# Kernel tuning notes

Hardware: AMD Instinct MI355X
Metric: run time of the kernel (lower is better)

The kernel has to match this reference:

```python
import jax, jax.numpy as jnp
import numpy as np

N_NODES = 100000
N_EDGES = 1600000
DIM_IN, DIM_H, DIM_OUT = 15, 128, 1


def _glorot(key, shape):
    fan_in, fan_out = shape[0], shape[1]
    lim = float(np.sqrt(6.0 / (fan_in + fan_out)))
    return jax.random.uniform(key, shape, jnp.float32, -lim, lim)


def setup_inputs() -> dict:
    key = jax.random.key(0)
    ks = jax.random.split(key, 12)
    x = jax.random.normal(ks[0], (N_NODES, DIM_IN), jnp.float32)
    edge_index = jax.random.randint(ks[1], (2, N_EDGES), 0, N_NODES, jnp.int64)
    # PyG SAGEConv: out = lin_l(mean_aggr(x_src)) + lin_r(x_dst); bias lives in lin_l.
    # Weights stored as [in, out] for x @ W.
    params = {
        "W1l": _glorot(ks[2], (DIM_IN, DIM_H)), "W1r": _glorot(ks[3], (DIM_IN, DIM_H)), "b1": jnp.zeros((DIM_H,), jnp.float32),
        "W2l": _glorot(ks[4], (DIM_H, DIM_H)), "W2r": _glorot(ks[5], (DIM_H, DIM_H)), "b2": jnp.zeros((DIM_H,), jnp.float32),
        "W3l": _glorot(ks[6], (DIM_H, DIM_OUT)), "W3r": _glorot(ks[7], (DIM_H, DIM_OUT)), "b3": jnp.zeros((DIM_OUT,), jnp.float32),
    }
    return {"x": x, "edge_index": edge_index, **params}


def _sage_conv(h, src, dst, deg_inv, Wl, Wr, b):
    # mean-aggregate source features at destination nodes
    agg = jax.ops.segment_sum(h[src], dst, num_segments=N_NODES) * deg_inv
    return agg @ Wl + h @ Wr + b


def reference(x, edge_index, W1l, W1r, b1, W2l, W2r, b2, W3l, W3r, b3):
    src, dst = edge_index[0], edge_index[1]
    deg = jax.ops.segment_sum(jnp.ones((src.shape[0],), x.dtype), dst, num_segments=N_NODES)
    deg_inv = (1.0 / jnp.maximum(deg, 1.0))[:, None]  # [N,1]
    h = jax.nn.relu(_sage_conv(x, src, dst, deg_inv, W1l, W1r, b1))  # dropout is identity in eval
    h = jax.nn.relu(_sage_conv(h, src, dst, deg_inv, W2l, W2r, b2))
    h = _sage_conv(h, src, dst, deg_inv, W3l, W3r, b3)
    return h
```

## Files before the change

kernel.cpp:

```cpp
#include <hip/hip_runtime.h>
#include <hip/hip_bf16.h>

constexpr int N = 100000;
constexpr int E = 1600000;
constexpr int DIN = 15;
constexpr int DH  = 128;
constexpr int K2  = 256;
constexpr int NPAD = 100032;

constexpr int CHUNK     = 8192;
constexpr int NBLK_P1   = (E + CHUNK - 1) / CHUNK;
constexpr int BKT_NODES = 512;
constexpr int NBKT      = (N + BKT_NODES - 1) / BKT_NODES;
constexpr int LREC_CAP  = 10240;

typedef short short8 __attribute__((ext_vector_type(8)));
typedef float f32x4  __attribute__((ext_vector_type(4)));

__device__ __forceinline__ unsigned short f2bf_rne(float f) {
    unsigned u = __float_as_uint(f);
    u += 0x7fffu + ((u >> 16) & 1u);
    return (unsigned short)(u >> 16);
}
__device__ __forceinline__ float bf2f(unsigned short h) {
    return __uint_as_float(((unsigned)h) << 16);
}
__device__ __forceinline__ float bflo(unsigned u) { return __uint_as_float(u << 16); }
__device__ __forceinline__ float bfhi(unsigned u) { return __uint_as_float(u & 0xffff0000u); }

__global__ __launch_bounds__(256) void k_prep(const float* __restrict__ x,
                                              const float* __restrict__ W2l,
                                              const float* __restrict__ W2r,
                                              const float* __restrict__ W1l,
                                              const float* __restrict__ W1r,
                                              unsigned int* __restrict__ xb32,
                                              unsigned short* __restrict__ Wthi,
                                              unsigned short* __restrict__ Wtlo,
                                              unsigned short* __restrict__ Wt1hi,
                                              unsigned short* __restrict__ Wt1lo,
                                              unsigned int* __restrict__ agg1b,
                                              int* __restrict__ btot) {
    int id = blockIdx.x * 256 + threadIdx.x;
    if (id < NBKT) btot[id] = 0;
    if (id < DH * K2) {
        int col = id & 127;
        int k   = id >> 7;
        float wv = (k < DH) ? W2l[k * DH + col] : W2r[(k - DH) * DH + col];
        unsigned short hi = f2bf_rne(wv);
        unsigned short lo = f2bf_rne(wv - bf2f(hi));
        Wthi[col * K2 + k] = hi;
        Wtlo[col * K2 + k] = lo;
        return;
    }
    int xid = id - DH * K2;
    if (xid < NPAD * 8) {
        int n = xid >> 3, d2 = xid & 7;
        unsigned v = 0;
        if (n < N) {
            int d0 = 2 * d2, d1 = 2 * d2 + 1;
            float v0 = x[n * DIN + d0];
            float v1 = (d1 < DIN) ? x[n * DIN + d1] : 0.f;
            v = (unsigned)f2bf_rne(v0) | ((unsigned)f2bf_rne(v1) << 16);
        }
        xb32[xid] = v;
        return;
    }
    int wid = xid - NPAD * 8;
    if (wid < DH * 32) {
        int col = wid >> 5;
        int k   = wid & 31;
        float wv = 0.f;
        if (k < DIN)                 wv = W1l[k * DH + col];
        else if (k >= 16 && k < 31)  wv = W1r[(k - 16) * DH + col];
        unsigned short hi = f2bf_rne(wv);
        unsigned short lo = f2bf_rne(wv - bf2f(hi));
        Wt1hi[col * 32 + k] = hi;
        Wt1lo[col * 32 + k] = lo;
        return;
    }
    int aid = wid - DH * 32;
    if (aid < (NPAD - N) * 8) agg1b[N * 8 + aid] = 0;
}

__global__ __launch_bounds__(1024) void k_p1(const int* __restrict__ src,
                                             const int* __restrict__ dst,
                                             unsigned int* __restrict__ bsorted,
                                             int* __restrict__ offg,
                                             int* __restrict__ btot) {
    __shared__ int hist[256];
    __shared__ int scn[256];
    __shared__ int fill[256];
    __shared__ unsigned int srt[CHUNK];
    const int t   = threadIdx.x;
    const int blk = blockIdx.x;
    const int e0  = blk * CHUNK;
    if (t < 256) hist[t] = 0;
    __syncthreads();
#pragma unroll
    for (int j = 0; j < CHUNK / 1024; ++j) {
        int i = e0 + t + j * 1024;
        if (i < E) atomicAdd(&hist[dst[i] >> 9], 1);
    }
    __syncthreads();
    if (t < 256) {
        if (t < NBKT && hist[t]) atomicAdd(&btot[t], hist[t]);
        scn[t] = hist[t];
    }
    __syncthreads();
    for (int d = 1; d < 256; d <<= 1) {
        int v = (t >= d && t < 256) ? scn[t - d] : 0;
        __syncthreads();
        if (t < 256) scn[t] += v;
        __syncthreads();
    }
    if (t < 256) {
        int excl = (t == 0) ? 0 : scn[t - 1];
        fill[t] = excl;
        if (t < NBKT) offg[blk * (NBKT + 1) + t] = excl;
        if (t == 0)   offg[blk * (NBKT + 1) + NBKT] = scn[NBKT - 1];
    }
    __syncthreads();
#pragma unroll
    for (int j = 0; j < CHUNK / 1024; ++j) {
        int i = e0 + t + j * 1024;
        if (i < E) {
            int dv = dst[i];
            int b  = dv >> 9;
            int pos = atomicAdd(&fill[b], 1);
            srt[pos] = ((unsigned)(dv & 511) << 17) | (unsigned)src[i];
        }
    }
    __syncthreads();
    for (int i = t; i < CHUNK; i += 1024) bsorted[e0 + i] = srt[i];
}

__global__ __launch_bounds__(1024) void k_p2(const unsigned int* __restrict__ bsorted,
                                             const int* __restrict__ offg,
                                             const int* __restrict__ btot,
                                             int* __restrict__ csr,
                                             int* __restrict__ rowptr,
                                             float* __restrict__ deg_inv) {
    __shared__ unsigned int lrec[LREC_CAP];
    __shared__ int cum[NBLK_P1 + 1];
    __shared__ int runstart[NBLK_P1];
    __shared__ int ldeg[BKT_NODES];
    __shared__ int lrp[BKT_NODES];
    __shared__ int lfill[BKT_NODES];
    __shared__ int pscan[256];
    __shared__ int sbs;

    const int b = blockIdx.x;
    const int t = threadIdx.x;

    if (t < 256) pscan[t] = (t < NBKT) ? btot[t] : 0;
    __syncthreads();
    for (int d = 1; d < 256; d <<= 1) {
        int v = (t >= d && t < 256) ? pscan[t - d] : 0;
        __syncthreads();
        if (t < 256) pscan[t] += v;
        __syncthreads();
    }
    if (t == 0) sbs = (b == 0) ? 0 : pscan[b - 1];
    __syncthreads();
    const int bs = sbs;

    int cnt_blk = 0;
    if (t < NBLK_P1) {
        int o0 = offg[t * (NBKT + 1) + b];
        cnt_blk = offg[t * (NBKT + 1) + b + 1] - o0;
        runstart[t] = o0;
    }
    __syncthreads();
    if (t < 256) pscan[t] = cnt_blk;
    __syncthreads();
    for (int d = 1; d < 256; d <<= 1) {
        int v = (t >= d && t < 256) ? pscan[t - d] : 0;
        __syncthreads();
        if (t < 256) pscan[t] += v;
        __syncthreads();
    }
    if (t < NBLK_P1) cum[t] = (t == 0) ? 0 : pscan[t - 1];
    if (t == 0) cum[NBLK_P1] = pscan[NBLK_P1 - 1];
    if (t < BKT_NODES) ldeg[t] = 0;
    __syncthreads();

    int total = cum[NBLK_P1];
    if (total > LREC_CAP) total = LREC_CAP;

    for (int i = t; i < total; i += 1024) {
        int lo = 0, hi = NBLK_P1;
        while (hi - lo > 1) {
            int mid = (lo + hi) >> 1;
            if (cum[mid] <= i) lo = mid; else hi = mid;
        }
        lrec[i] = bsorted[lo * CHUNK + runstart[lo] + (i - cum[lo])];
    }
    __syncthreads();

    for (int i = t; i < total; i += 1024) atomicAdd(&ldeg[lrec[i] >> 17], 1);
    __syncthreads();

    int p0 = 0, p1 = 0;
    if (t < 256) {
        p0 = ldeg[2 * t];
        p1 = ldeg[2 * t + 1];
        pscan[t] = p0 + p1;
    }
    __syncthreads();
    for (int d = 1; d < 256; d <<= 1) {
        int v = (t >= d && t < 256) ? pscan[t - d] : 0;
        __syncthreads();
        if (t < 256) pscan[t] += v;
        __syncthreads();
    }
    if (t < 256) {
        int pairbase = (t == 0) ? 0 : pscan[t - 1];
        lrp[2 * t]     = pairbase;
        lrp[2 * t + 1] = pairbase + p0;
    }
    if (t < BKT_NODES) lfill[t] = 0;
    __syncthreads();

    for (int i = t; i < total; i += 1024) {
        unsigned rec = lrec[i];
        int ld  = rec >> 17;
        int pos = lrp[ld] + atomicAdd(&lfill[ld], 1);
        csr[bs + pos] = (int)(rec & 0x1ffff);
    }
    if (t < BKT_NODES) {
        int g = b * BKT_NODES + t;
        if (g < N) {
            rowptr[g]  = bs + lrp[t];
            deg_inv[g] = 1.0f / fmaxf((float)ldeg[t], 1.0f);
        }
    }
    if (b == NBKT - 1 && t == 0) rowptr[N] = E;
}

__global__ __launch_bounds__(256) void k_agg1(const int* __restrict__ rowptr,
                                              const int* __restrict__ csr,
                                              const uint2* __restrict__ xb2,
                                              const float* __restrict__ deg_inv,
                                              uint2* __restrict__ agg1b2) {
    const int tid = threadIdx.x;
    const int l4  = tid & 3;
    const int gb4 = (tid & 63) & 60;
    const int n = blockIdx.x * 64 + (tid >> 2);
    if (n >= N) return;
    const int lo = rowptr[n], hi = rowptr[n + 1];
    float a0 = 0.f, a1 = 0.f, a2 = 0.f, a3 = 0.f;
    float b0 = 0.f, b1 = 0.f, b2 = 0.f, b3 = 0.f;
    float c0 = 0.f, c1 = 0.f, c2 = 0.f, c3 = 0.f;
    float d0 = 0.f, d1 = 0.f, d2 = 0.f, d3 = 0.f;
    int base = lo;
    for (; base + 8 <= hi; base += 8) {
        int e0 = csr[base + l4];
        int e1 = csr[base + 4 + l4];
        int s0 = __shfl(e0, gb4 + 0), s1 = __shfl(e0, gb4 + 1);
        int s2 = __shfl(e0, gb4 + 2), s3 = __shfl(e0, gb4 + 3);
        int s4 = __shfl(e1, gb4 + 0), s5 = __shfl(e1, gb4 + 1);
        int s6 = __shfl(e1, gb4 + 2), s7 = __shfl(e1, gb4 + 3);
        uint2 u0 = xb2[s0 * 4 + l4];
        uint2 u1 = xb2[s1 * 4 + l4];
        uint2 u2 = xb2[s2 * 4 + l4];
        uint2 u3 = xb2[s3 * 4 + l4];
        uint2 u4 = xb2[s4 * 4 + l4];
        uint2 u5 = xb2[s5 * 4 + l4];
        uint2 u6 = xb2[s6 * 4 + l4];
        uint2 u7 = xb2[s7 * 4 + l4];
        a0 += bflo(u0.x); a1 += bfhi(u0.x); a2 += bflo(u0.y); a3 += bfhi(u0.y);
        b0 += bflo(u1.x); b1 += bfhi(u1.x); b2 += bflo(u1.y); b3 += bfhi(u1.y);
        c0 += bflo(u2.x); c1 += bfhi(u2.x); c2 += bflo(u2.y); c3 += bfhi(u2.y);
        d0 += bflo(u3.x); d1 += bfhi(u3.x); d2 += bflo(u3.y); d3 += bfhi(u3.y);
        a0 += bflo(u4.x); a1 += bfhi(u4.x); a2 += bflo(u4.y); a3 += bfhi(u4.y);
        b0 += bflo(u5.x); b1 += bfhi(u5.x); b2 += bflo(u5.y); b3 += bfhi(u5.y);
        c0 += bflo(u6.x); c1 += bfhi(u6.x); c2 += bflo(u6.y); c3 += bfhi(u6.y);
        d0 += bflo(u7.x); d1 += bfhi(u7.x); d2 += bflo(u7.y); d3 += bfhi(u7.y);
    }
    int cnt = hi - base;
    if (cnt > 0) {
        int e0 = (base + l4 < hi) ? csr[base + l4] : 0;
        int e1 = (base + 4 + l4 < hi) ? csr[base + 4 + l4] : 0;
        int jm = min(cnt, 4);
        for (int j = 0; j < jm; ++j) {
            int s = __shfl(e0, gb4 + j);
            uint2 u = xb2[s * 4 + l4];
            a0 += bflo(u.x); a1 += bfhi(u.x); a2 += bflo(u.y); a3 += bfhi(u.y);
        }
        for (int j = 4; j < cnt; ++j) {
            int s = __shfl(e1, gb4 + j - 4);
            uint2 u = xb2[s * 4 + l4];
            b0 += bflo(u.x); b1 += bfhi(u.x); b2 += bflo(u.y); b3 += bfhi(u.y);
        }
    }
    const float di = deg_inv[n];
    float v0 = ((a0 + b0) + (c0 + d0)) * di;
    float v1 = ((a1 + b1) + (c1 + d1)) * di;
    float v2 = ((a2 + b2) + (c2 + d2)) * di;
    float v3 = ((a3 + b3) + (c3 + d3)) * di;
    uint2 o;
    o.x = (unsigned)f2bf_rne(v0) | ((unsigned)f2bf_rne(v1) << 16);
    o.y = (unsigned)f2bf_rne(v2) | ((unsigned)f2bf_rne(v3) << 16);
    agg1b2[n * 4 + l4] = o;
}

__global__ __launch_bounds__(256) void k_h1(const uint4* __restrict__ agg1b4,
                                            const uint4* __restrict__ xb4,
                                            const unsigned short* __restrict__ Wt1hi,
                                            const unsigned short* __restrict__ Wt1lo,
                                            const float* __restrict__ b1,
                                            unsigned int* __restrict__ h1hi32) {
    __shared__ __align__(16) unsigned short sA[4 * 64 * 8];
    __shared__ __align__(16) unsigned short sH[64 * 128];
    __shared__ float sb[DH];

    const int tid   = threadIdx.x;
    const int node0 = blockIdx.x * 64;

    if (tid < DH) sb[tid] = b1[tid];
    {
        int c = tid >> 6;
        int n = tid & 63;
        uint4 v = (c < 2) ? agg1b4[(node0 + n) * 2 + c]
                          : xb4[(node0 + n) * 2 + (c - 2)];
        *(uint4*)&sA[(c * 64 + (n ^ c)) * 8] = v;
    }
    __syncthreads();

    const int w    = tid >> 6;
    const int lane = tid & 63;
    const int cg   = lane & 15;
    const int lg   = lane >> 4;

    f32x4 acc[4][2];
#pragma unroll
    for (int a = 0; a < 4; ++a)
#pragma unroll
        for (int b = 0; b < 2; ++b)
            acc[a][b] = (f32x4){0.f, 0.f, 0.f, 0.f};

    short8 bh0 = *(const short8*)&Wt1hi[(w * 32 + 0 * 16 + cg) * 32 + lg * 8];
    short8 bh1 = *(const short8*)&Wt1hi[(w * 32 + 1 * 16 + cg) * 32 + lg * 8];
    short8 bl0 = *(const short8*)&Wt1lo[(w * 32 + 0 * 16 + cg) * 32 + lg * 8];
    short8 bl1 = *(const short8*)&Wt1lo[(w * 32 + 1 * 16 + cg) * 32 + lg * 8];

#pragma unroll
    for (int rt = 0; rt < 4; ++rt) {
        const int n = rt * 16 + cg;
        short8 a = *(const short8*)&sA[(lg * 64 + (n ^ lg)) * 8];
        acc[rt][0] = __builtin_amdgcn_mfma_f32_16x16x32_bf16(a, bh0, acc[rt][0], 0, 0, 0);
        acc[rt][0] = __builtin_amdgcn_mfma_f32_16x16x32_bf16(a, bl0, acc[rt][0], 0, 0, 0);
        acc[rt][1] = __builtin_amdgcn_mfma_f32_16x16x32_bf16(a, bh1, acc[rt][1], 0, 0, 0);
        acc[rt][1] = __builtin_amdgcn_mfma_f32_16x16x32_bf16(a, bl1, acc[rt][1], 0, 0, 0);
    }

#pragma unroll
    for (int rt = 0; rt < 4; ++rt)
#pragma unroll
        for (int ci = 0; ci < 2; ++ci) {
            const int col = w * 32 + ci * 16 + cg;
            const float bb = sb[col];
#pragma unroll
            for (int reg = 0; reg < 4; ++reg) {
                const int row = rt * 16 + lg * 4 + reg;
                sH[row * 128 + col] = f2bf_rne(fmaxf(acc[rt][ci][reg] + bb, 0.f));
            }
        }
    __syncthreads();
    const uint4* sH4 = (const uint4*)sH;
    uint4* out4 = (uint4*)h1hi32;
#pragma unroll
    for (int it = 0; it < 4; ++it) {
        int idx = tid + it * 256;
        out4[node0 * 16 + idx] = sH4[idx];
    }
}

__global__ __launch_bounds__(256) void k_agg2(const int* __restrict__ rowptr,
                                              const int* __restrict__ csr,
                                              const unsigned int* __restrict__ h1b,
                                              const float* __restrict__ deg_inv,
                                              unsigned int* __restrict__ agg2b) {
    const int lane = threadIdx.x & 63;
    const int n = blockIdx.x * 4 + (threadIdx.x >> 6);
    if (n >= N) return;
    const int lo = rowptr[n], hi = rowptr[n + 1];
    float a0x = 0.f, a0y = 0.f, a1x = 0.f, a1y = 0.f;
    float a2x = 0.f, a2y = 0.f, a3x = 0.f, a3y = 0.f;
    float a4x = 0.f, a4y = 0.f, a5x = 0.f, a5y = 0.f;
    float a6x = 0.f, a6y = 0.f, a7x = 0.f, a7y = 0.f;
    for (int base = lo; base < hi; base += 64) {
        const int cnt = min(64, hi - base);
        int e = (base + lane < hi) ? csr[base + lane] : 0;
        int j = 0;
        for (; j + 8 <= cnt; j += 8) {
            int s0 = __shfl(e, j + 0), s1 = __shfl(e, j + 1);
            int s2 = __shfl(e, j + 2), s3 = __shfl(e, j + 3);
            int s4 = __shfl(e, j + 4), s5 = __shfl(e, j + 5);
            int s6 = __shfl(e, j + 6), s7 = __shfl(e, j + 7);
            unsigned u0 = h1b[s0 * 64 + lane];
            unsigned u1 = h1b[s1 * 64 + lane];
            unsigned u2 = h1b[s2 * 64 + lane];
            unsigned u3 = h1b[s3 * 64 + lane];
            unsigned u4 = h1b[s4 * 64 + lane];
            unsigned u5 = h1b[s5 * 64 + lane];
            unsigned u6 = h1b[s6 * 64 + lane];
            unsigned u7 = h1b[s7 * 64 + lane];
            a0x += bflo(u0); a0y += bfhi(u0);
            a1x += bflo(u1); a1y += bfhi(u1);
            a2x += bflo(u2); a2y += bfhi(u2);
            a3x += bflo(u3); a3y += bfhi(u3);
            a4x += bflo(u4); a4y += bfhi(u4);
            a5x += bflo(u5); a5y += bfhi(u5);
            a6x += bflo(u6); a6y += bfhi(u6);
            a7x += bflo(u7); a7y += bfhi(u7);
        }
        for (; j < cnt; ++j) {
            int s = __shfl(e, j);
            unsigned u = h1b[s * 64 + lane];
            a0x += bflo(u); a0y += bfhi(u);
        }
    }
    const float di = deg_inv[n];
    float vx = (((a0x + a1x) + (a2x + a3x)) + ((a4x + a5x) + (a6x + a7x))) * di;
    float vy = (((a0y + a1y) + (a2y + a3y)) + ((a4y + a5y) + (a6y + a7y))) * di;
    agg2b[n * 64 + lane] = (unsigned)f2bf_rne(vx) | ((unsigned)f2bf_rne(vy) << 16);
}

__global__ __launch_bounds__(256) void k_h2pr(const unsigned int* __restrict__ agg2b,
                                              const unsigned int* __restrict__ h1hi32,
                                              const unsigned short* __restrict__ Wthi,
                                              const unsigned short* __restrict__ Wtlo,
                                              const float* __restrict__ b2,
                                              const float* __restrict__ W3l,
                                              const float* __restrict__ W3r,
                                              float* __restrict__ p,
                                              float* __restrict__ r) {
    __shared__ __align__(16) unsigned short sA[32 * 64 * 8];
    __shared__ float sb2[DH], sW3l[DH], sW3r[DH];
    __shared__ float sPP[4 * 64], sPR[4 * 64];

    const int tid   = threadIdx.x;
    const int node0 = blockIdx.x * 64;

    if (tid < DH) {
        sb2[tid]  = b2[tid];
        sW3l[tid] = W3l[tid];
        sW3r[tid] = W3r[tid];
    }

#pragma unroll
    for (int it = 0; it < 4; ++it) {
        int idx = tid + it * 256;
        int n   = idx >> 4;
        int cp  = idx & 15;
        uint4 va = *(const uint4*)&agg2b[(node0 + n) * 64 + cp * 4];
        *(uint4*)&sA[(cp * 64 + (n ^ (cp & 7))) * 8] = va;
    }
#pragma unroll
    for (int it = 0; it < 4; ++it) {
        int idx = tid + it * 256;
        int n   = idx >> 4;
        int cp  = idx & 15;
        int c   = 16 + cp;
        uint4 vh = *(const uint4*)&h1hi32[(node0 + n) * 64 + cp * 4];
        *(uint4*)&sA[(c * 64 + (n ^ (cp & 7))) * 8] = vh;
    }
    __syncthreads();

    const int w    = tid >> 6;
    const int lane = tid & 63;
    const int cg   = lane & 15;
    const int lg   = lane >> 4;

    f32x4 acc[4][2];
#pragma unroll
    for (int a = 0; a < 4; ++a)
#pragma unroll
        for (int b = 0; b < 2; ++b)
            acc[a][b] = (f32x4){0.f, 0.f, 0.f, 0.f};

    const unsigned short* bhp0 = &Wthi[(w * 32 + 0 * 16 + cg) * K2 + lg * 8];
    const unsigned short* bhp1 = &Wthi[(w * 32 + 1 * 16 + cg) * K2 + lg * 8];
    const unsigned short* blp0 = &Wtlo[(w * 32 + 0 * 16 + cg) * K2 + lg * 8];
    const unsigned short* blp1 = &Wtlo[(w * 32 + 1 * 16 + cg) * K2 + lg * 8];

#pragma unroll
    for (int s = 0; s < 8; ++s) {
        short8 a[4];
#pragma unroll
        for (int rt = 0; rt < 4; ++rt) {
            const int c = s * 4 + lg;
            const int n = rt * 16 + cg;
            a[rt] = *(const short8*)&sA[(c * 64 + (n ^ (c & 7))) * 8];
        }
        short8 bhi0 = *(const short8*)(bhp0 + s * 32);
        short8 bhi1 = *(const short8*)(bhp1 + s * 32);
        short8 blo0 = *(const short8*)(blp0 + s * 32);
        short8 blo1 = *(const short8*)(blp1 + s * 32);
#pragma unroll
        for (int rt = 0; rt < 4; ++rt) {
            acc[rt][0] = __builtin_amdgcn_mfma_f32_16x16x32_bf16(a[rt], bhi0, acc[rt][0], 0, 0, 0);
            acc[rt][0] = __builtin_amdgcn_mfma_f32_16x16x32_bf16(a[rt], blo0, acc[rt][0], 0, 0, 0);
            acc[rt][1] = __builtin_amdgcn_mfma_f32_16x16x32_bf16(a[rt], bhi1, acc[rt][1], 0, 0, 0);
            acc[rt][1] = __builtin_amdgcn_mfma_f32_16x16x32_bf16(a[rt], blo1, acc[rt][1], 0, 0, 0);
        }
    }

    float pl[4][4] = {{0.f}}, rl[4][4] = {{0.f}};
#pragma unroll
    for (int rt = 0; rt < 4; ++rt)
#pragma unroll
        for (int ci = 0; ci < 2; ++ci) {
            const int col = w * 32 + ci * 16 + cg;
            const float bb = sb2[col], w3l = sW3l[col], w3r = sW3r[col];
#pragma unroll
            for (int reg = 0; reg < 4; ++reg) {
                float h2v = fmaxf(acc[rt][ci][reg] + bb, 0.f);
                pl[rt][reg] = fmaf(h2v, w3l, pl[rt][reg]);
                rl[rt][reg] = fmaf(h2v, w3r, rl[rt][reg]);
            }
        }
#pragma unroll
    for (int m = 8; m >= 1; m >>= 1)
#pragma unroll
        for (int rt = 0; rt < 4; ++rt)
#pragma unroll
            for (int reg = 0; reg < 4; ++reg) {
                pl[rt][reg] += __shfl_xor(pl[rt][reg], m, 64);
                rl[rt][reg] += __shfl_xor(rl[rt][reg], m, 64);
            }
    if (cg == 0) {
#pragma unroll
        for (int rt = 0; rt < 4; ++rt)
#pragma unroll
            for (int reg = 0; reg < 4; ++reg) {
                const int row = rt * 16 + lg * 4 + reg;
                sPP[w * 64 + row] = pl[rt][reg];
                sPR[w * 64 + row] = rl[rt][reg];
            }
    }
    __syncthreads();
    if (tid < 64) {
        float sp = sPP[tid] + sPP[64 + tid] + sPP[128 + tid] + sPP[192 + tid];
        float sr = sPR[tid] + sPR[64 + tid] + sPR[128 + tid] + sPR[192 + tid];
        p[node0 + tid] = sp;
        r[node0 + tid] = sr;
    }
}

__global__ __launch_bounds__(256) void k_out(const int* __restrict__ rowptr,
                                             const int* __restrict__ csr,
                                             const float* __restrict__ p,
                                             const float* __restrict__ r,
                                             const float* __restrict__ deg_inv,
                                             const float* __restrict__ b3,
                                             float* __restrict__ out) {
    const int tid = threadIdx.x;
    const int l7  = tid & 7;
    const int n   = blockIdx.x * 32 + (tid >> 3);
    if (n >= N) return;
    const int lo = rowptr[n], hi = rowptr[n + 1];
    float a = 0.f, b = 0.f;
    int i = lo + l7;
    for (; i + 8 < hi; i += 16) {
        a += p[csr[i]];
        b += p[csr[i + 8]];
    }
    if (i < hi) a += p[csr[i]];
    a += b;
    a += __shfl_xor(a, 1, 64);
    a += __shfl_xor(a, 2, 64);
    a += __shfl_xor(a, 4, 64);
    if (l7 == 0) out[n] = a * deg_inv[n] + r[n] + b3[0];
}

extern "C" void kernel_launch(void* const* d_in, const int* in_sizes, int n_in,
                              void* d_out, int out_size, void* d_ws, size_t ws_size,
                              hipStream_t stream) {
    const float* x    = (const float*)d_in[0];
    const int*   eidx = (const int*)d_in[1];
    const float* W1l  = (const float*)d_in[2];
    const float* W1r  = (const float*)d_in[3];
    const float* b1   = (const float*)d_in[4];
    const float* W2l  = (const float*)d_in[5];
    const float* W2r  = (const float*)d_in[6];
    const float* b2   = (const float*)d_in[7];
    const float* W3l  = (const float*)d_in[8];
    const float* W3r  = (const float*)d_in[9];
    const float* b3   = (const float*)d_in[10];
    float* out = (float*)d_out;

    const int* srcs = eidx;
    const int* dsts = eidx + E;

    size_t off = 0;
    auto alloc = [&](size_t bytes) {
        size_t o = off;
        off = (off + bytes + 255) & ~(size_t)255;
        return o;
    };
    char* w = (char*)d_ws;
    int*   rowptr  = (int*)(w + alloc((size_t)(N + 1) * 4));
    int*   csr     = (int*)(w + alloc((size_t)E * 4));
    float* deg_inv = (float*)(w + alloc((size_t)N * 4));
    unsigned int* xb32   = (unsigned int*)(w + alloc((size_t)NPAD * 8 * 4));
    unsigned int* agg1b  = (unsigned int*)(w + alloc((size_t)NPAD * 8 * 4));
    unsigned short* h1hi = (unsigned short*)(w + alloc((size_t)NPAD * DH * 2));
    unsigned int* agg2b  = (unsigned int*)(w + alloc((size_t)NPAD * 64 * 4));
    float* pbuf    = (float*)(w + alloc((size_t)NPAD * 4));
    float* rbuf    = (float*)(w + alloc((size_t)NPAD * 4));
    unsigned short* Wthi  = (unsigned short*)(w + alloc((size_t)DH * K2 * 2));
    unsigned short* Wtlo  = (unsigned short*)(w + alloc((size_t)DH * K2 * 2));
    unsigned short* Wt1hi = (unsigned short*)(w + alloc((size_t)DH * 32 * 2));
    unsigned short* Wt1lo = (unsigned short*)(w + alloc((size_t)DH * 32 * 2));
    unsigned int* bsorted = (unsigned int*)(w + alloc((size_t)NBLK_P1 * CHUNK * 4));
    int*   offg    = (int*)(w + alloc((size_t)NBLK_P1 * (NBKT + 1) * 4));
    int*   btot    = (int*)(w + alloc((size_t)NBKT * 4));
    (void)ws_size;

    const int prep_ids = DH * K2 + NPAD * 8 + DH * 32 + (NPAD - N) * 8;

    k_prep<<<(prep_ids + 255) / 256, 256, 0, stream>>>(x, W2l, W2r, W1l, W1r, xb32,
                                                       Wthi, Wtlo, Wt1hi, Wt1lo,
                                                       agg1b, btot);
    k_p1<<<NBLK_P1, 1024, 0, stream>>>(srcs, dsts, bsorted, offg, btot);
    k_p2<<<NBKT, 1024, 0, stream>>>(bsorted, offg, btot, csr, rowptr, deg_inv);

    k_agg1<<<(N + 63) / 64, 256, 0, stream>>>(rowptr, csr, (const uint2*)xb32,
                                              deg_inv, (uint2*)agg1b);
    k_h1<<<NPAD / 64, 256, 0, stream>>>((const uint4*)agg1b, (const uint4*)xb32,
                                        Wt1hi, Wt1lo, b1, (unsigned int*)h1hi);

    k_agg2<<<(N + 3) / 4, 256, 0, stream>>>(rowptr, csr, (const unsigned int*)h1hi,
                                            deg_inv, agg2b);

    k_h2pr<<<NPAD / 64, 256, 0, stream>>>(agg2b, (const unsigned int*)h1hi,
                                          Wthi, Wtlo, b2, W3l, W3r, pbuf, rbuf);

    k_out<<<(N + 31) / 32, 256, 0, stream>>>(rowptr, csr, pbuf, rbuf, deg_inv, b3, out);
}
```

Baseline: 173.0 us.

## Merge prep and edge-bucketing kernels, deepen layer-2 gather unroll

```diff
diff --git a/kernel.cpp b/kernel.cpp
--- a/kernel.cpp
+++ b/kernel.cpp
@@ -14,6 +14,9 @@
 constexpr int NBKT      = (N + BKT_NODES - 1) / BKT_NODES;
 constexpr int LREC_CAP  = 10240;
 
+constexpr int PREP_IDS    = DH * K2 + NPAD * 8 + DH * 32 + (NPAD - N) * 8;
+constexpr int PREP_BLOCKS = (PREP_IDS + 1023) / 1024;
+
 typedef short short8 __attribute__((ext_vector_type(8)));
 typedef float f32x4  __attribute__((ext_vector_type(4)));
 
@@ -28,7 +31,12 @@
 __device__ __forceinline__ float bflo(unsigned u) { return __uint_as_float(u << 16); }
 __device__ __forceinline__ float bfhi(unsigned u) { return __uint_as_float(u & 0xffff0000u); }
 
-__global__ __launch_bounds__(256) void k_prep(const float* __restrict__ x,
+__global__ __launch_bounds__(1024) void k_pre(const int* __restrict__ src,
+                                              const int* __restrict__ dst,
+                                              unsigned int* __restrict__ bsorted,
+                                              int* __restrict__ offg,
+                                              int* __restrict__ btot,
+                                              const float* __restrict__ x,
                                               const float* __restrict__ W2l,
                                               const float* __restrict__ W2r,
                                               const float* __restrict__ W1l,
@@ -38,60 +46,56 @@
                                               unsigned short* __restrict__ Wtlo,
                                               unsigned short* __restrict__ Wt1hi,
                                               unsigned short* __restrict__ Wt1lo,
-                                              unsigned int* __restrict__ agg1b,
-                                              int* __restrict__ btot) {
-    int id = blockIdx.x * 256 + threadIdx.x;
-    if (id < NBKT) btot[id] = 0;
-    if (id < DH * K2) {
-        int col = id & 127;
-        int k   = id >> 7;
-        float wv = (k < DH) ? W2l[k * DH + col] : W2r[(k - DH) * DH + col];
-        unsigned short hi = f2bf_rne(wv);
-        unsigned short lo = f2bf_rne(wv - bf2f(hi));
-        Wthi[col * K2 + k] = hi;
-        Wtlo[col * K2 + k] = lo;
-        return;
-    }
-    int xid = id - DH * K2;
-    if (xid < NPAD * 8) {
-        int n = xid >> 3, d2 = xid & 7;
-        unsigned v = 0;
-        if (n < N) {
-            int d0 = 2 * d2, d1 = 2 * d2 + 1;
-            float v0 = x[n * DIN + d0];
-            float v1 = (d1 < DIN) ? x[n * DIN + d1] : 0.f;
-            v = (unsigned)f2bf_rne(v0) | ((unsigned)f2bf_rne(v1) << 16);
-        }
-        xb32[xid] = v;
-        return;
-    }
-    int wid = xid - NPAD * 8;
-    if (wid < DH * 32) {
-        int col = wid >> 5;
-        int k   = wid & 31;
-        float wv = 0.f;
-        if (k < DIN)                 wv = W1l[k * DH + col];
-        else if (k >= 16 && k < 31)  wv = W1r[(k - 16) * DH + col];
-        unsigned short hi = f2bf_rne(wv);
-        unsigned short lo = f2bf_rne(wv - bf2f(hi));
-        Wt1hi[col * 32 + k] = hi;
-        Wt1lo[col * 32 + k] = lo;
-        return;
-    }
-    int aid = wid - DH * 32;
-    if (aid < (NPAD - N) * 8) agg1b[N * 8 + aid] = 0;
-}
-
-__global__ __launch_bounds__(1024) void k_p1(const int* __restrict__ src,
-                                             const int* __restrict__ dst,
-                                             unsigned int* __restrict__ bsorted,
-                                             int* __restrict__ offg,
-                                             int* __restrict__ btot) {
+                                              unsigned int* __restrict__ agg1b) {
     __shared__ int hist[256];
     __shared__ int scn[256];
     __shared__ int fill[256];
     __shared__ unsigned int srt[CHUNK];
-    const int t   = threadIdx.x;
+    const int t = threadIdx.x;
+
+    if (blockIdx.x >= NBLK_P1) {
+        int id = (blockIdx.x - NBLK_P1) * 1024 + t;
+        if (id < DH * K2) {
+            int col = id & 127;
+            int k   = id >> 7;
+            float wv = (k < DH) ? W2l[k * DH + col] : W2r[(k - DH) * DH + col];
+            unsigned short hi = f2bf_rne(wv);
+            unsigned short lo = f2bf_rne(wv - bf2f(hi));
+            Wthi[col * K2 + k] = hi;
+            Wtlo[col * K2 + k] = lo;
+            return;
+        }
+        int xid = id - DH * K2;
+        if (xid < NPAD * 8) {
+            int n = xid >> 3, d2 = xid & 7;
+            unsigned v = 0;
+            if (n < N) {
+                int d0 = 2 * d2, d1 = 2 * d2 + 1;
+                float v0 = x[n * DIN + d0];
+                float v1 = (d1 < DIN) ? x[n * DIN + d1] : 0.f;
+                v = (unsigned)f2bf_rne(v0) | ((unsigned)f2bf_rne(v1) << 16);
+            }
+            xb32[xid] = v;
+            return;
+        }
+        int wid = xid - NPAD * 8;
+        if (wid < DH * 32) {
+            int col = wid >> 5;
+            int k   = wid & 31;
+            float wv = 0.f;
+            if (k < DIN)                 wv = W1l[k * DH + col];
+            else if (k >= 16 && k < 31)  wv = W1r[(k - 16) * DH + col];
+            unsigned short hi = f2bf_rne(wv);
+            unsigned short lo = f2bf_rne(wv - bf2f(hi));
+            Wt1hi[col * 32 + k] = hi;
+            Wt1lo[col * 32 + k] = lo;
+            return;
+        }
+        int aid = wid - DH * 32;
+        if (aid < (NPAD - N) * 8) agg1b[N * 8 + aid] = 0;
+        return;
+    }
+
     const int blk = blockIdx.x;
     const int e0  = blk * CHUNK;
     if (t < 256) hist[t] = 0;
@@ -393,7 +397,49 @@
         const int cnt = min(64, hi - base);
         int e = (base + lane < hi) ? csr[base + lane] : 0;
         int j = 0;
-        for (; j + 8 <= cnt; j += 8) {
+        for (; j + 16 <= cnt; j += 16) {
+            int s0 = __shfl(e, j + 0),  s1 = __shfl(e, j + 1);
+            int s2 = __shfl(e, j + 2),  s3 = __shfl(e, j + 3);
+            int s4 = __shfl(e, j + 4),  s5 = __shfl(e, j + 5);
+            int s6 = __shfl(e, j + 6),  s7 = __shfl(e, j + 7);
+            int s8 = __shfl(e, j + 8),  s9 = __shfl(e, j + 9);
+            int s10 = __shfl(e, j + 10), s11 = __shfl(e, j + 11);
+            int s12 = __shfl(e, j + 12), s13 = __shfl(e, j + 13);
+            int s14 = __shfl(e, j + 14), s15 = __shfl(e, j + 15);
+            unsigned u0  = h1b[s0 * 64 + lane];
+            unsigned u1  = h1b[s1 * 64 + lane];
+            unsigned u2  = h1b[s2 * 64 + lane];
+            unsigned u3  = h1b[s3 * 64 + lane];
+            unsigned u4  = h1b[s4 * 64 + lane];
+            unsigned u5  = h1b[s5 * 64 + lane];
+            unsigned u6  = h1b[s6 * 64 + lane];
+            unsigned u7  = h1b[s7 * 64 + lane];
+            unsigned u8  = h1b[s8 * 64 + lane];
+            unsigned u9  = h1b[s9 * 64 + lane];
+            unsigned u10 = h1b[s10 * 64 + lane];
+            unsigned u11 = h1b[s11 * 64 + lane];
+            unsigned u12 = h1b[s12 * 64 + lane];
+            unsigned u13 = h1b[s13 * 64 + lane];
+            unsigned u14 = h1b[s14 * 64 + lane];
+            unsigned u15 = h1b[s15 * 64 + lane];
+            a0x += bflo(u0);  a0y += bfhi(u0);
+            a1x += bflo(u1);  a1y += bfhi(u1);
+            a2x += bflo(u2);  a2y += bfhi(u2);
+            a3x += bflo(u3);  a3y += bfhi(u3);
+            a4x += bflo(u4);  a4y += bfhi(u4);
+            a5x += bflo(u5);  a5y += bfhi(u5);
+            a6x += bflo(u6);  a6y += bfhi(u6);
+            a7x += bflo(u7);  a7y += bfhi(u7);
+            a0x += bflo(u8);  a0y += bfhi(u8);
+            a1x += bflo(u9);  a1y += bfhi(u9);
+            a2x += bflo(u10); a2y += bfhi(u10);
+            a3x += bflo(u11); a3y += bfhi(u11);
+            a4x += bflo(u12); a4y += bfhi(u12);
+            a5x += bflo(u13); a5y += bfhi(u13);
+            a6x += bflo(u14); a6y += bfhi(u14);
+            a7x += bflo(u15); a7y += bfhi(u15);
+        }
+        if (j + 8 <= cnt) {
             int s0 = __shfl(e, j + 0), s1 = __shfl(e, j + 1);
             int s2 = __shfl(e, j + 2), s3 = __shfl(e, j + 3);
             int s4 = __shfl(e, j + 4), s5 = __shfl(e, j + 5);
@@ -414,6 +460,7 @@
             a5x += bflo(u5); a5y += bfhi(u5);
             a6x += bflo(u6); a6y += bfhi(u6);
             a7x += bflo(u7); a7y += bfhi(u7);
+            j += 8;
         }
         for (; j < cnt; ++j) {
             int s = __shfl(e, j);
@@ -619,12 +666,10 @@
     int*   btot    = (int*)(w + alloc((size_t)NBKT * 4));
     (void)ws_size;
 
-    const int prep_ids = DH * K2 + NPAD * 8 + DH * 32 + (NPAD - N) * 8;
-
-    k_prep<<<(prep_ids + 255) / 256, 256, 0, stream>>>(x, W2l, W2r, W1l, W1r, xb32,
-                                                       Wthi, Wtlo, Wt1hi, Wt1lo,
-                                                       agg1b, btot);
-    k_p1<<<NBLK_P1, 1024, 0, stream>>>(srcs, dsts, bsorted, offg, btot);
+    hipMemsetAsync(btot, 0, (size_t)NBKT * 4, stream);
+    k_pre<<<NBLK_P1 + PREP_BLOCKS, 1024, 0, stream>>>(srcs, dsts, bsorted, offg, btot,
+                                                      x, W2l, W2r, W1l, W1r, xb32,
+                                                      Wthi, Wtlo, Wt1hi, Wt1lo, agg1b);
     k_p2<<<NBKT, 1024, 0, stream>>>(bsorted, offg, btot, csr, rowptr, deg_inv);
 
     k_agg1<<<(N + 63) / 64, 256, 0, stream>>>(rowptr, csr, (const uint2*)xb32,
```

Result: slower. 181.8 us (+5.1%).
